# Performance work log

Hardware: AMD Instinct MI355X
Metric: run time of the kernel (lower is better)

## Reference

```python
import jax, jax.numpy as jnp
import numpy as np
import math

B, C, H, W = 16, 256, 32, 32
MPHI = 16      # GRModule projection channels
NNODE = 20     # symbol nodes
DEMB = 300     # fastText dim


def setup_inputs() -> dict:
    key = jax.random.key(0)
    ks = jax.random.split(key, 24)
    r = lambda i, shp, s=0.05: jax.random.normal(ks[i], shp, dtype=jnp.float32) * s
    return {
        'x': r(0, (B, C, H, W), 1.0),
        'emb': r(1, (NNODE, DEMB), 1.0),
        'adj': jax.random.uniform(ks[2], (NNODE, NNODE), dtype=jnp.float32),
        'wq': r(3, (DEMB, DEMB)), 'bq': r(4, (DEMB,)),
        'wk': r(5, (DEMB, DEMB)), 'bk': r(6, (DEMB,)),
        'wv': r(7, (DEMB, DEMB)), 'bv': r(8, (DEMB,)),
        'wo': r(9, (DEMB, DEMB)), 'bo': r(10, (DEMB,)),
        'phi_w': r(11, (MPHI, C)), 'phi_b': r(12, (MPHI,)),
        'glob_w': r(13, (MPHI, C)),
        'gc1_w': r(14, (DEMB, C)),
        'gc2_w': r(15, (C, C)),
        'gw_w': r(16, (C, C)),
        's2l_w': r(17, (2 * C,)), 's2l_b': r(18, (1,)),
        'final_w': r(19, (C, 2 * C)),
    }


def _attention_graph(node, wq, bq, wk, bk, wv, bv, wo, bo):
    # node: [N, 300]. Single-head self-attention, mean-pooled residual (dropout=eval).
    q = node @ wq + bq
    k = node @ wk + bk
    v = node @ wv + bv
    att = jax.nn.softmax(q @ k.T / math.sqrt(DEMB), axis=-1)
    node1 = (att @ v).mean(axis=0, keepdims=True)      # [1, 300]
    node2 = node1 @ wo + bo
    return node + node2                                 # broadcast residual


def _gr_module(x, phi_w, phi_b, glob_w):
    # x: [B, C, H, W] -> [B, HW, C]
    b = x.shape[0]
    phi = jnp.einsum('oc,bchw->bohw', phi_w, x) + phi_b[None, :, None, None]  # [B,16,H,W]
    x_phi = jax.nn.relu(phi.reshape(b, -1, MPHI))       # raw reshape, as in torch .view
    x_phi_T = jax.nn.relu(phi.reshape(b, MPHI, -1))
    g = jnp.einsum('oc,bc->bo', glob_w, x.mean(axis=(2, 3)))  # [B,16]
    # sigmoid of the diag-embedded matrix: off-diagonal becomes sigmoid(0)=0.5 (faithful)
    Dg = jax.nn.sigmoid(jax.vmap(jnp.diag)(g))          # [B,16,16]
    A = jax.nn.softmax(jnp.einsum('bpm,bmn,bnq->bpq', x_phi, Dg, x_phi_T), axis=-1)
    d = 1.0 / jnp.sqrt(A.sum(axis=2))
    d = jnp.where(jnp.isfinite(d), d, 0.0)              # nan/inf -> 0
    L = jnp.eye(A.shape[1], dtype=A.dtype) - d[:, :, None] * A * d[:, None, :]
    return jnp.einsum('bpq,bqc->bpc', L, x.reshape(b, -1, x.shape[1]))


def _normalize_adjacency(adj):
    a_hat = adj + jnp.eye(adj.shape[0], dtype=adj.dtype)
    d = 1.0 / jnp.sqrt(a_hat.sum(axis=1))
    d = jnp.where(jnp.isfinite(d), d, 0.0)
    return d[:, None] * a_hat * d[None, :]


def reference(x, emb, adj, wq, bq, wk, bk, wv, bv, wo, bo,
              phi_w, phi_b, glob_w, gc1_w, gc2_w, gw_w, s2l_w, s2l_b, final_w):
    b, c, h, w = x.shape
    # --- semantic branch: attention over word graph + 2-layer GCN ---
    ev = _attention_graph(emb, wq, bq, wk, bk, wv, bv, wo, bo)  # [N,300]
    ev = jnp.broadcast_to(ev[None], (b, NNODE, DEMB))
    adj_n = _normalize_adjacency(adj)                   # [N,N]
    g1 = jax.nn.relu(jnp.einsum('pq,bqd->bpd', adj_n, ev @ gc1_w))   # [B,N,256]
    g2 = jax.nn.relu(jnp.einsum('pq,bqd->bpd', adj_n, g1 @ gc2_w))   # [B,N,256]
    # --- local branch: GRModule Laplacian smoothing + 1x1 conv ---
    spiral = _gr_module(x, phi_w, phi_b, glob_w)        # [B,HW,C]
    spiral_map = spiral.reshape(b, h, w, c).transpose(0, 3, 1, 2)    # [B,C,H,W]
    local = jnp.einsum('oc,bchw->bohw', gw_w, spiral_map)
    # --- semantic-to-local mapping (1x1 conv over concat == two dot products) ---
    inp_flat = x.transpose(0, 2, 3, 1).reshape(b, h * w, c)          # [B,HW,C]
    w_in, w_ev = s2l_w[:c], s2l_w[c:]
    logits = (inp_flat @ w_in)[:, :, None] + (g2 @ w_ev)[:, None, :] + s2l_b[0]
    mapping = jax.nn.softmax(logits, axis=1)            # softmax over pixels
    app = jax.nn.relu(jnp.einsum('bpm,bmc->bpc', mapping, g2))       # [B,HW,C]
    app = app.reshape(b, h, w, c).transpose(0, 3, 1, 2)              # [B,C,H,W]
    # --- fuse ---
    fused = jnp.concatenate([local, app], axis=1)       # [B,2C,H,W]
    out = jnp.einsum('oc,bchw->bohw', final_w, fused)
    return jax.nn.relu(out + x)
```

## Files before the change

kernel.cpp:

```cpp
#include <hip/hip_runtime.h>
#include <hip/hip_bf16.h>

typedef __bf16 bf16_t;
typedef bf16_t bf16x8 __attribute__((ext_vector_type(8)));
typedef bf16_t bf16x4 __attribute__((ext_vector_type(4)));
typedef float  f32x4  __attribute__((ext_vector_type(4)));

#define MFMA(a,b,c) __builtin_amdgcn_mfma_f32_16x16x32_bf16((a),(b),(c),0,0,0)

__global__ __launch_bounds__(256) void k_front(
    const float* final_w, const float* gw_w, const float* emb,
    const float* wq, const float* bq, const float* wk, const float* bk,
    const float* wv, const float* bvv, const float* x,
    const float* phi_w, const float* phi_b, const float* s2l_w,
    const float* gc1_w, const float* wo, const float* bo,
    bf16_t* M16, float* qkv, bf16_t* fB, bf16_t* fBT, float* s_raw,
    float* xsump, float* csum, float* fmaxp, float* cmaxp, bf16_t* xT,
    float* E1, float* WG1, float* bg1) {
  __shared__ __align__(16) char sp[27648];
  int bid = blockIdx.x, t = threadIdx.x;
  if (bid < 256) {
    float* fw = (float*)sp;
    int o = bid, c = t;
    fw[c] = final_w[o*512 + c];
    __syncthreads();
    float acc = 0.f;
    for (int k = 0; k < 256; ++k) acc += fw[k] * gw_w[k*256 + c];
    M16[o*256 + c] = (bf16_t)acc;
    return;
  }
  if (bid < 316) {
    int id = bid - 256;
    int mat = id / 20, row = id % 20;
    const float* W  = mat == 0 ? wq : (mat == 1 ? wk : wv);
    const float* Bb = mat == 0 ? bq : (mat == 1 ? bk : bvv);
    float* er = (float*)sp;
    for (int i = t; i < 300; i += 256) er[i] = emb[row*300 + i];
    __syncthreads();
    for (int o = t; o < 300; o += 256) {
      float acc = Bb[o];
      for (int d = 0; d < 300; ++d) acc += er[d] * W[d*300 + o];
      qkv[(mat*20 + row)*300 + o] = acc;
    }
    return;
  }
  if (bid < 444) {
    int id = bid - 316;
    int b = id >> 3, role = id & 7;
    const float* xb = x + b*262144;
    float* pw = (float*)sp;
    float* wi = pw + 4096;
    float* pb = wi + 256;
    float* phs = pb + 16;
    unsigned* fmu = (unsigned*)(phs + 2304);
    unsigned* cmu = fmu + 16;
    for (int i = t; i < 4096; i += 256) pw[i] = phi_w[i];
    wi[t] = s2l_w[t];
    if (t < 16) { pb[t] = phi_b[t]; fmu[t] = 0u; }
    if (t == 0) cmu[0] = 0u;
    __syncthreads();
    int hwl = t & 127, half = t >> 7;
    int hw = role*128 + hwl;
    float ph[16];
    #pragma unroll
    for (int o = 0; o < 16; ++o) ph[o] = 0.f;
    float sacc = 0.f;
    for (int ci = 0; ci < 128; ++ci) {
      int c = half*128 + ci;
      float xv = xb[c*1024 + hw];
      sacc += wi[c] * xv;
      #pragma unroll
      for (int o = 0; o < 16; ++o) ph[o] += pw[o*256 + c] * xv;
    }
    if (half == 0) {
      #pragma unroll
      for (int o = 0; o < 16; ++o) phs[hwl*18 + o] = ph[o];
      phs[hwl*18 + 16] = sacc;
    }
    __syncthreads();
    if (half == 1) {
      #pragma unroll
      for (int o = 0; o < 16; ++o) phs[hwl*18 + o] += ph[o];
      s_raw[b*1024 + hw] = phs[hwl*18 + 16] + sacc;
    }
    __syncthreads();
    float csacc = 0.f;
    #pragma unroll
    for (int i = 0; i < 8; ++i) {
      int j = i*256 + t;
      int o = j >> 7, hl = j & 127;
      float val = fmaxf(phs[hl*18 + o] + pb[o], 0.f);
      bf16_t bv16 = (bf16_t)val;
      atomicMax(&fmu[o], __float_as_uint((float)bv16));
      fB [b*16384 + o*1024 + role*128 + hl] = bv16;
      fBT[b*16384 + (role*128 + hl)*16 + o] = bv16;
      csacc += (float)bv16;
    }
    if (half == 0) phs[hwl*18 + 17] = csacc;
    __syncthreads();
    if (half == 1) {
      float cs = phs[hwl*18 + 17] + csacc;
      csum[b*1024 + hw] = cs;
      atomicMax(cmu, __float_as_uint(cs));
    }
    if (t < 16) fmaxp[b*128 + role*16 + t] = __uint_as_float(fmu[t]);
    __syncthreads();
    if (t == 0) cmaxp[b*8 + role] = __uint_as_float(cmu[0]);
    {
      const f32x4* xr = (const f32x4*)(xb + t*1024 + role*128);
      float s4 = 0.f;
      #pragma unroll
      for (int j = 0; j < 32; ++j) { f32x4 v = xr[j]; s4 += v[0] + v[1] + v[2] + v[3]; }
      xsump[(b*8 + role)*256 + t] = s4;
    }
    return;
  }
  if (bid < 464) {
    int n = bid - 444;
    float* er = (float*)sp;
    for (int i = t; i < 300; i += 256) er[i] = emb[n*300 + i];
    __syncthreads();
    float acc = 0.f;
    for (int d = 0; d < 300; ++d) acc += er[d] * gc1_w[d*256 + t];
    E1[n*256 + t] = acc;
    return;
  }
  if (bid < 765) {
    int d0 = bid - 464;
    float* er = (float*)sp;
    if (d0 < 300) { for (int i = t; i < 300; i += 256) er[i] = wo[d0*300 + i]; }
    else          { for (int i = t; i < 300; i += 256) er[i] = bo[i]; }
    __syncthreads();
    float acc = 0.f;
    for (int e = 0; e < 300; ++e) acc += er[e] * gc1_w[e*256 + t];
    if (d0 < 300) WG1[d0*256 + t] = acc; else bg1[t] = acc;
    return;
  }
  {
    int id = bid - 765;
    int bb = id >> 6, tile = id & 63;
    int q0 = (tile >> 2) * 64, c0 = (tile & 3) * 64;
    bf16_t* tl = (bf16_t*)sp;
    const float* xbb = x + bb*262144;
    #pragma unroll
    for (int k = 0; k < 16; ++k) {
      int idx = k*256 + t, qi = idx >> 6, ci = idx & 63;
      tl[ci*74 + qi] = (bf16_t)xbb[(q0 + qi)*256 + c0 + ci];
    }
    __syncthreads();
    #pragma unroll
    for (int k = 0; k < 16; ++k) {
      int idx = k*256 + t, ci = idx >> 6, qi = idx & 63;
      xT[bb*262144 + (c0 + ci)*1024 + q0 + qi] = tl[ci*74 + qi];
    }
    return;
  }
}

__global__ __launch_bounds__(512) void k_mid1(
    const float* adj, const float* qkv, const float* E1,
    const float* glob_w, const float* xsump, const float* s_raw,
    const float* fmaxp, const float* cmaxp,
    float* n1g, float* adjng, float* rsAg, float* AE1g,
    float* dgd, float* mcol, float* fmaxb, float* cmaxb) {
  __shared__ __align__(16) float sp[12480];
  int t = threadIdx.x;
  if (blockIdx.x == 0) {
    float* A  = sp;
    float* Bs = A + 6000;
    float* att  = Bs + 6000;
    float* wsum = att + 400;
    for (int i = t; i < 6000; i += 512) { A[i] = qkv[i]; Bs[i] = qkv[6000 + i]; }
    __syncthreads();
    if (t < 400) {
      int i = t / 20, j = t % 20;
      float acc = 0.f;
      for (int d = 0; d < 300; ++d) acc += A[i*300 + d] * Bs[j*300 + d];
      att[t] = acc * 0.05773502691896258f;
    }
    __syncthreads();
    if (t < 20) {
      float m = -1e30f;
      for (int j = 0; j < 20; ++j) m = fmaxf(m, att[t*20 + j]);
      float s = 0.f;
      for (int j = 0; j < 20; ++j) { float e = __expf(att[t*20 + j] - m); att[t*20 + j] = e; s += e; }
      float inv = 1.f / s;
      for (int j = 0; j < 20; ++j) att[t*20 + j] *= inv;
    }
    __syncthreads();
    if (t < 20) {
      float s = 0.f;
      for (int i = 0; i < 20; ++i) s += att[i*20 + t];
      wsum[t] = s * 0.05f;
    }
    __syncthreads();
    if (t < 300) {
      const float* v = qkv + 12000;
      float acc = 0.f;
      for (int j = 0; j < 20; ++j) acc += wsum[j] * v[j*300 + t];
      n1g[t] = acc;
    }
    return;
  }
  if (blockIdx.x == 1) {
    float* drt = sp;
    float* an  = sp + 32;
    if (t < 20) {
      float s = 1.f;
      for (int j = 0; j < 20; ++j) s += adj[t*20 + j];
      drt[t] = rsqrtf(s);
    }
    __syncthreads();
    if (t < 400) {
      int i = t / 20, j = t % 20;
      float a = adj[t] + (i == j ? 1.f : 0.f);
      float v = drt[i] * a * drt[j];
      an[t] = v;
      adjng[t] = v;
    }
    __syncthreads();
    if (t < 20) {
      float s = 0.f;
      for (int m = 0; m < 20; ++m) s += an[t*20 + m];
      rsAg[t] = s;
    }
    if (t < 256) {
      float e[20];
      #pragma unroll
      for (int m = 0; m < 20; ++m) e[m] = E1[m*256 + t];
      for (int n = 0; n < 20; ++n) {
        float acc = 0.f;
        #pragma unroll
        for (int m = 0; m < 20; ++m) acc += an[n*20 + m] * e[m];
        AE1g[n*256 + t] = acc;
      }
    }
    return;
  }
  int b = blockIdx.x - 2;
  float* xm = sp;
  float* redm = xm + 256;
  float* reds = redm + 8;
  if (t < 256) {
    float s = 0.f;
    #pragma unroll
    for (int r = 0; r < 8; ++r) s += xsump[(b*8 + r)*256 + t];
    xm[t] = s * (1.f / 1024.f);
  }
  if (t >= 256 && t < 272) {
    int m = t - 256; float fm = 0.f;
    for (int r = 0; r < 8; ++r) fm = fmaxf(fm, fmaxp[b*128 + r*16 + m]);
    fmaxb[b*16 + m] = fm;
  }
  if (t == 272) {
    float cm = 0.f;
    for (int r = 0; r < 8; ++r) cm = fmaxf(cm, cmaxp[b*8 + r]);
    cmaxb[b] = cm;
  }
  __syncthreads();
  if (t < 16) {
    float g = 0.f;
    for (int c = 0; c < 256; ++c) g += glob_w[t*256 + c] * xm[c];
    dgd[b*16 + t] = 0.5f * tanhf(0.5f * g);
  }
  float v0 = s_raw[b*1024 + t], v1 = s_raw[b*1024 + 512 + t];
  float m = fmaxf(v0, v1);
  #pragma unroll
  for (int off = 32; off; off >>= 1) m = fmaxf(m, __shfl_xor(m, off, 64));
  int wv = t >> 6, ll = t & 63;
  if (ll == 0) redm[wv] = m;
  __syncthreads();
  float bm = redm[0];
  #pragma unroll
  for (int i = 1; i < 8; ++i) bm = fmaxf(bm, redm[i]);
  float e0 = __expf(v0 - bm), e1 = __expf(v1 - bm);
  float s2 = e0 + e1;
  #pragma unroll
  for (int off = 32; off; off >>= 1) s2 += __shfl_xor(s2, off, 64);
  if (ll == 0) reds[wv] = s2;
  __syncthreads();
  float tot = 0.f;
  #pragma unroll
  for (int i = 0; i < 8; ++i) tot += reds[i];
  float inv = 1.f / tot;
  mcol[b*1024 + t]       = e0 * inv;
  mcol[b*1024 + 512 + t] = e1 * inv;
}

__global__ __launch_bounds__(256) void k_w1(const float* n1g, const float* WG1,
                                            float* w1part) {
  int t = threadIdx.x, i = blockIdx.x, d0 = i*8;
  float acc = 0.f;
  #pragma unroll
  for (int k = 0; k < 8; ++k) {
    int d = d0 + k;
    if (d < 300) acc += n1g[d] * WG1[d*256 + t];
  }
  w1part[i*256 + t] = acc;
}

__global__ __launch_bounds__(256) void k_gu(const float* w1part,
    const float* bg1, const float* AE1g, const float* rsAg, const float* adjng,
    const float* gc2_w, const float* final_w, float* upart) {
  __shared__ float adjns[400], rsAs[32], w1s[256], h2s[176], rgs[8];
  __shared__ float g1s[20*260];
  __shared__ float gs2[2048];
  int t = threadIdx.x, c0 = blockIdx.x * 8;
  for (int i = t; i < 400; i += 256) adjns[i] = adjng[i];
  if (t < 20) rsAs[t] = rsAg[t];
  #pragma unroll
  for (int k2 = 0; k2 < 8; ++k2) {
    int idx = k2*256 + t, d = idx >> 3, cl = idx & 7;
    gs2[idx] = gc2_w[d*256 + c0 + cl];
  }
  {
    float acc = bg1[t];
    #pragma unroll
    for (int i = 0; i < 38; ++i) acc += w1part[i*256 + t];
    w1s[t] = acc;
  }
  float ae[20];
  #pragma unroll
  for (int k2 = 0; k2 < 20; ++k2) ae[k2] = AE1g[k2*256 + t];
  __syncthreads();
  #pragma unroll
  for (int k2 = 0; k2 < 20; ++k2)
    g1s[k2*260 + t] = fmaxf(ae[k2] + rsAs[k2] * w1s[t], 0.f);
  __syncthreads();
  int cl = t & 7, n = t >> 3;
  if (n < 20) {
    float acc = 0.f;
    for (int d = 0; d < 256; ++d) acc += g1s[n*260 + d] * gs2[d*8 + cl];
    h2s[n*8 + cl] = acc;
  }
  __syncthreads();
  if (t < 8) {
    float rga = 0.f;
    for (int nn = 0; nn < 20; ++nn) {
      float a2 = 0.f;
      #pragma unroll
      for (int m = 0; m < 20; ++m) a2 += adjns[nn*20 + m] * h2s[m*8 + t];
      rga += fmaxf(a2, 0.f);
    }
    rgs[t] = rga;
  }
  __syncthreads();
  {
    float acc = 0.f;
    const float* fw = final_w + t*512 + 256 + c0;
    #pragma unroll
    for (int kk = 0; kk < 8; ++kk) acc += fw[kk] * rgs[kk];
    upart[blockIdx.x*256 + t] = acc;
  }
}

__global__ __launch_bounds__(256) void k_main(const float* x, const bf16_t* fB,
    const bf16_t* fBT, const bf16_t* xT, const bf16_t* M16, const float* fmaxb,
    const float* mcol, const float* upart, const float* dgd, const float* csum,
    const float* cmaxb, float* out) {
  int flat = blockIdx.y * 32 + blockIdx.x;
  int b  = (flat & 7) * 2 + ((flat >> 3) >> 5);
  int p0 = ((flat >> 3) & 31) * 32;
  int t = threadIdx.x, w = t >> 6, l = t & 63, lr = l & 15, quad = l >> 4;
  int ph = w & 1, ch = w >> 1;
  __shared__ __align__(16) char smem[16896];
  bf16_t* e_s  = (bf16_t*)smem;
  bf16_t* T_ls = (bf16_t*)smem;
  __shared__ float Mb_s[32], fmax_s[16], u_s[256], dgd_s[16];
  __shared__ float c_s[1024], ha_s[32];
  const float*  xb   = x   + b*262144;
  const bf16_t* fBb  = fB  + b*16384;
  const bf16_t* fBTb = fBT + b*16384;
  const bf16_t* xTb  = xT  + b*262144;
  for (int i = t; i < 1280; i += 256) e_s[i] = (bf16_t)0.f;
  {
    float us = 0.f;
    #pragma unroll
    for (int j = 0; j < 32; ++j) us += upart[j*256 + t];
    u_s[t] = us;
  }
  for (int i = t; i < 1024; i += 256) c_s[i] = csum[b*1024 + i];
  if (t < 16) { fmax_s[t] = fmaxb[b*16 + t]; dgd_s[t] = dgd[b*16 + t]; }
  __syncthreads();
  for (int i = t; i < 512; i += 256) {
    int p = i >> 4, m = i & 15;
    e_s[p*40 + m] = (bf16_t)((float)fBb[p0*16 + i] * dgd_s[m]);
  }
  __syncthreads();
  if (t < 32) {
    float a = 0.f;
    #pragma unroll
    for (int m = 0; m < 16; ++m) a += (float)fBb[(p0 + t)*16 + m];
    float ha = 0.5f * a;
    ha_s[t] = ha;
    float mb = ha * cmaxb[b];
    #pragma unroll
    for (int m = 0; m < 16; ++m) mb += fmaxf((float)e_s[t*40 + m], 0.f) * fmax_s[m];
    Mb_s[t] = mb;
  }
  __syncthreads();
  bf16x8 be = *(const bf16x8*)(e_s + (ph*16 + lr)*40 + quad*8);
  float mb_lane = Mb_s[ph*16 + lr];
  float ha_lane = ha_s[ph*16 + lr];
  float rs = 0.f;
  f32x4 acc[8];
  #pragma unroll
  for (int j = 0; j < 8; ++j) acc[j] = (f32x4){0.f, 0.f, 0.f, 0.f};
  bf16x8 zer;
  #pragma unroll
  for (int j = 0; j < 8; ++j) zer[j] = (bf16_t)0.f;
  const bf16_t* xrow = xTb + (ch*128 + lr)*1024 + quad*8;
  int srcLo = ((quad & 1) << 5) + lr;
  int srcHi = srcLo + 16;
  bool hi = quad >= 2;
  for (int st = 0; st < 32; ++st) {
    bf16x8 a0 = zer, a1 = zer;
    if (quad < 2) {
      a0 = *(const bf16x8*)(fBTb + (st*32 + lr)*16 + quad*8);
      a1 = *(const bf16x8*)(fBTb + (st*32 + 16 + lr)*16 + quad*8);
    }
    bf16x8 bv[8];
    #pragma unroll
    for (int cf = 0; cf < 8; ++cf)
      bv[cf] = *(const bf16x8*)(xrow + cf*16384 + st*32);
    f32x4 z = {0.f, 0.f, 0.f, 0.f};
    f32x4 s0 = MFMA(a0, be, z);
    f32x4 s1 = MFMA(a1, be, z);
    float E0[4], E1v[4];
    #pragma unroll
    for (int r = 0; r < 4; ++r) {
      float S0 = s0[r] + ha_lane * c_s[st*32 + quad*4 + r];
      float S1 = s1[r] + ha_lane * c_s[st*32 + 16 + quad*4 + r];
      E0[r] = __expf(S0 - mb_lane);
      E1v[r] = __expf(S1 - mb_lane);
      rs += E0[r] + E1v[r];
    }
    unsigned P0, P1, P2, P3;
    {
      union { bf16_t h[2]; unsigned u; } pk;
      pk.h[0] = (bf16_t)E0[0];  pk.h[1] = (bf16_t)E0[1];  P0 = pk.u;
      pk.h[0] = (bf16_t)E0[2];  pk.h[1] = (bf16_t)E0[3];  P1 = pk.u;
      pk.h[0] = (bf16_t)E1v[0]; pk.h[1] = (bf16_t)E1v[1]; P2 = pk.u;
      pk.h[0] = (bf16_t)E1v[2]; pk.h[1] = (bf16_t)E1v[3]; P3 = pk.u;
    }
    unsigned xA = (unsigned)__shfl((int)P0, srcLo, 64);
    unsigned xB = (unsigned)__shfl((int)P2, srcLo, 64);
    unsigned yA = (unsigned)__shfl((int)P1, srcLo, 64);
    unsigned yB = (unsigned)__shfl((int)P3, srcLo, 64);
    unsigned zA = (unsigned)__shfl((int)P0, srcHi, 64);
    unsigned zB = (unsigned)__shfl((int)P2, srcHi, 64);
    unsigned wA = (unsigned)__shfl((int)P1, srcHi, 64);
    unsigned wB = (unsigned)__shfl((int)P3, srcHi, 64);
    union { unsigned u[4]; bf16x8 v; } af;
    af.u[0] = hi ? xB : xA;
    af.u[1] = hi ? yB : yA;
    af.u[2] = hi ? zB : zA;
    af.u[3] = hi ? wB : wA;
    bf16x8 ap = af.v;
    #pragma unroll
    for (int cf = 0; cf < 8; ++cf) acc[cf] = MFMA(ap, bv[cf], acc[cf]);
  }
  rs += __shfl_xor(rs, 16, 64);
  rs += __shfl_xor(rs, 32, 64);
  float rsinv = 1.f / fmaxf(rs, 1e-30f);
  float rsv[4];
  #pragma unroll
  for (int r = 0; r < 4; ++r) rsv[r] = __shfl(rsinv, quad*4 + r, 64);
  __syncthreads();
  #pragma unroll
  for (int cf = 0; cf < 8; ++cf)
    #pragma unroll
    for (int r = 0; r < 4; ++r) {
      int p = ph*16 + quad*4 + r;
      int c = ch*128 + cf*16 + lr;
      float tv = xb[(p0 + p)*256 + c] - acc[cf][r] * rsv[r];
      T_ls[p*264 + c] = (bf16_t)tv;
    }
  __syncthreads();
  f32x4 acc2[4][2];
  #pragma unroll
  for (int i = 0; i < 4; ++i)
    #pragma unroll
    for (int j = 0; j < 2; ++j) acc2[i][j] = (f32x4){0.f, 0.f, 0.f, 0.f};
  for (int c0 = 0; c0 < 256; c0 += 32) {
    bf16x8 am[4], bt[2];
    #pragma unroll
    for (int of = 0; of < 4; ++of)
      am[of] = *(const bf16x8*)(M16 + (w*64 + of*16 + lr)*256 + c0 + quad*8);
    #pragma unroll
    for (int pf = 0; pf < 2; ++pf)
      bt[pf] = *(const bf16x8*)(T_ls + (pf*16 + lr)*264 + c0 + quad*8);
    #pragma unroll
    for (int of = 0; of < 4; ++of)
      #pragma unroll
      for (int pf = 0; pf < 2; ++pf) acc2[of][pf] = MFMA(am[of], bt[pf], acc2[of][pf]);
  }
  float* outb = out + b*262144;
  #pragma unroll
  for (int of = 0; of < 4; ++of)
    #pragma unroll
    for (int pf = 0; pf < 2; ++pf)
      #pragma unroll
      for (int r = 0; r < 4; ++r) {
        int o = w*64 + of*16 + quad*4 + r;
        int pg = p0 + pf*16 + lr;
        float v = acc2[of][pf][r] + mcol[b*1024 + pg] * u_s[o] + xb[o*1024 + pg];
        outb[o*1024 + pg] = fmaxf(v, 0.f);
      }
}


extern "C" void kernel_launch(void* const* d_in, const int* in_sizes, int n_in,
                              void* d_out, int out_size, void* d_ws, size_t ws_size,
                              hipStream_t stream) {
  (void)in_sizes; (void)n_in; (void)out_size; (void)ws_size;
  const float* x       = (const float*)d_in[0];
  const float* emb     = (const float*)d_in[1];
  const float* adj     = (const float*)d_in[2];
  const float* wq      = (const float*)d_in[3];
  const float* bq      = (const float*)d_in[4];
  const float* wk      = (const float*)d_in[5];
  const float* bk      = (const float*)d_in[6];
  const float* wv      = (const float*)d_in[7];
  const float* bv      = (const float*)d_in[8];
  const float* wo      = (const float*)d_in[9];
  const float* bo      = (const float*)d_in[10];
  const float* phi_w   = (const float*)d_in[11];
  const float* phi_b   = (const float*)d_in[12];
  const float* glob_w  = (const float*)d_in[13];
  const float* gc1_w   = (const float*)d_in[14];
  const float* gc2_w   = (const float*)d_in[15];
  const float* gw_w    = (const float*)d_in[16];
  const float* s2l_w   = (const float*)d_in[17];
  const float* final_w = (const float*)d_in[19];
  float* out = (float*)d_out;

  float* W = (float*)d_ws;
  float* qkv    = W + 0;
  float* xsump  = W + 18048;
  float* s_raw  = W + 50816;
  float* mcol   = W + 67200;
  float* fmaxb  = W + 83584;
  float* dgd    = W + 83840;
  float* csum   = W + 84096;
  float* cmaxb  = W + 100480;
  float* fmaxp  = W + 100544;
  float* cmaxp  = W + 102592;
  float* E1     = W + 102720;
  float* WG1    = W + 107840;
  float* bg1    = W + 184640;
  float* n1     = W + 184896;
  float* adjn   = W + 185216;
  float* rsA    = W + 185664;
  float* AE1    = W + 185728;
  float* upart  = W + 190848;
  float* w1part = W + 199040;
  bf16_t* M16 = (bf16_t*)((char*)d_ws + 851968);
  bf16_t* fB  = (bf16_t*)((char*)d_ws + 983040);
  bf16_t* fBT = (bf16_t*)((char*)d_ws + 1507328);
  bf16_t* xT  = (bf16_t*)((char*)d_ws + 2031616);

  k_front<<<1789, 256, 0, stream>>>(final_w, gw_w, emb, wq, bq, wk, bk, wv, bv, x,
                                    phi_w, phi_b, s2l_w, gc1_w, wo, bo,
                                    M16, qkv, fB, fBT, s_raw, xsump, csum,
                                    fmaxp, cmaxp, xT, E1, WG1, bg1);
  k_mid1<<<18, 512, 0, stream>>>(adj, qkv, E1, glob_w, xsump, s_raw,
                                 fmaxp, cmaxp,
                                 n1, adjn, rsA, AE1, dgd, mcol, fmaxb, cmaxb);
  k_w1<<<38, 256, 0, stream>>>(n1, WG1, w1part);
  k_gu<<<32, 256, 0, stream>>>(w1part, bg1, AE1, rsA, adjn, gc2_w, final_w, upart);
  k_main<<<dim3(32, 16), 256, 0, stream>>>(x, fB, fBT, xT, M16, fmaxb, mcol, upart,
                                           dgd, csum, cmaxb, out);
}
```

Measured before the change: 228.9 us.

## Halve k_main pixel tile, split key dimension across waves with LDS exchange and prefetch

k_main now processes 16 query pixels per block instead of 32 and launches twice as many blocks. The four waves are split two ways: pairs of waves each compute the exp scores for alternating 32-pixel key chunks, and each wave owns 64 output channels. Scores go through a double-buffered LDS tile with a block barrier each step, replacing the cross-lane shuffle exchange. The next step's fBT and xT operands are prefetched into registers. The aim is more blocks for occupancy and less per-block work, at the cost of a __syncthreads per key step, a cross-wave row-sum reduction, and reloading M16 and xT in twice as many blocks.

```diff
diff --git a/kernel.cpp b/kernel.cpp
--- a/kernel.cpp
+++ b/kernel.cpp
@@ -358,21 +358,22 @@
     const bf16_t* fBT, const bf16_t* xT, const bf16_t* M16, const float* fmaxb,
     const float* mcol, const float* upart, const float* dgd, const float* csum,
     const float* cmaxb, float* out) {
-  int flat = blockIdx.y * 32 + blockIdx.x;
-  int b  = (flat & 7) * 2 + ((flat >> 3) >> 5);
-  int p0 = ((flat >> 3) & 31) * 32;
+  int flat = blockIdx.y * 64 + blockIdx.x;
+  int b  = (flat & 7) * 2 + ((flat >> 3) >> 6);
+  int p0 = ((flat >> 3) & 63) * 16;
   int t = threadIdx.x, w = t >> 6, l = t & 63, lr = l & 15, quad = l >> 4;
-  int ph = w & 1, ch = w >> 1;
-  __shared__ __align__(16) char smem[16896];
-  bf16_t* e_s  = (bf16_t*)smem;
+  int ks = w >> 1, qh = w & 1;
+  __shared__ __align__(16) char smem[8448];
+  bf16_t* PT0  = (bf16_t*)smem;
+  bf16_t* e_s  = (bf16_t*)(smem + 5120);
   bf16_t* T_ls = (bf16_t*)smem;
-  __shared__ float Mb_s[32], fmax_s[16], u_s[256], dgd_s[16];
-  __shared__ float c_s[1024], ha_s[32];
+  __shared__ float Mb_s[16], fmax_s[16], u_s[256], rsinv_s[16], dgd_s[16];
+  __shared__ float c_s[1024], ha_s[16], rs_s[4][16];
   const float*  xb   = x   + b*262144;
   const bf16_t* fBb  = fB  + b*16384;
   const bf16_t* fBTb = fBT + b*16384;
   const bf16_t* xTb  = xT  + b*262144;
-  for (int i = t; i < 1280; i += 256) e_s[i] = (bf16_t)0.f;
+  for (int i = t; i < 640; i += 256) e_s[i] = (bf16_t)0.f;
   {
     float us = 0.f;
     #pragma unroll
@@ -382,12 +383,9 @@
   for (int i = t; i < 1024; i += 256) c_s[i] = csum[b*1024 + i];
   if (t < 16) { fmax_s[t] = fmaxb[b*16 + t]; dgd_s[t] = dgd[b*16 + t]; }
   __syncthreads();
-  for (int i = t; i < 512; i += 256) {
-    int p = i >> 4, m = i & 15;
-    e_s[p*40 + m] = (bf16_t)((float)fBb[p0*16 + i] * dgd_s[m]);
-  }
-  __syncthreads();
-  if (t < 32) {
+  e_s[(t >> 4)*40 + (t & 15)] = (bf16_t)((float)fBb[p0*16 + t] * dgd_s[t & 15]);
+  __syncthreads();
+  if (t < 16) {
     float a = 0.f;
     #pragma unroll
     for (int m = 0; m < 16; ++m) a += (float)fBb[(p0 + t)*16 + m];
@@ -399,114 +397,105 @@
     Mb_s[t] = mb;
   }
   __syncthreads();
-  bf16x8 be = *(const bf16x8*)(e_s + (ph*16 + lr)*40 + quad*8);
-  float mb_lane = Mb_s[ph*16 + lr];
-  float ha_lane = ha_s[ph*16 + lr];
+  bf16x8 be = *(const bf16x8*)(e_s + lr*40 + quad*8);
+  float mb_lane = Mb_s[lr];
+  float ha_lane = ha_s[lr];
   float rs = 0.f;
-  f32x4 acc[8];
-  #pragma unroll
-  for (int j = 0; j < 8; ++j) acc[j] = (f32x4){0.f, 0.f, 0.f, 0.f};
+  f32x4 acc[4];
+  #pragma unroll
+  for (int j = 0; j < 4; ++j) acc[j] = (f32x4){0.f, 0.f, 0.f, 0.f};
   bf16x8 zer;
   #pragma unroll
   for (int j = 0; j < 8; ++j) zer[j] = (bf16_t)0.f;
-  const bf16_t* xrow = xTb + (ch*128 + lr)*1024 + quad*8;
-  int srcLo = ((quad & 1) << 5) + lr;
-  int srcHi = srcLo + 16;
-  bool hi = quad >= 2;
-  for (int st = 0; st < 32; ++st) {
-    bf16x8 a0 = zer, a1 = zer;
-    if (quad < 2) {
-      a0 = *(const bf16x8*)(fBTb + (st*32 + lr)*16 + quad*8);
-      a1 = *(const bf16x8*)(fBTb + (st*32 + 16 + lr)*16 + quad*8);
-    }
-    bf16x8 bv[8];
-    #pragma unroll
-    for (int cf = 0; cf < 8; ++cf)
-      bv[cf] = *(const bf16x8*)(xrow + cf*16384 + st*32);
+  bf16x8 a0 = zer, a0n = zer;
+  if (quad < 2) a0 = *(const bf16x8*)(fBTb + (ks*32 + qh*16 + lr)*16 + quad*8);
+  const bf16_t* xrow = xTb + (w*64 + lr)*1024 + quad*8;
+  bf16x8 bv[2][4], bvn[2][4];
+  #pragma unroll
+  for (int k = 0; k < 2; ++k)
+    #pragma unroll
+    for (int cf = 0; cf < 4; ++cf)
+      bv[k][cf] = *(const bf16x8*)(xrow + cf*16384 + k*32);
+  int cur = 0;
+  for (int u2 = 0; u2 < 16; ++u2) {
+    int st = u2*2 + ks;
     f32x4 z = {0.f, 0.f, 0.f, 0.f};
     f32x4 s0 = MFMA(a0, be, z);
-    f32x4 s1 = MFMA(a1, be, z);
-    float E0[4], E1v[4];
+    if (u2 < 15) {
+      if (quad < 2)
+        a0n = *(const bf16x8*)(fBTb + (((u2 + 1)*2 + ks)*32 + qh*16 + lr)*16 + quad*8);
+      #pragma unroll
+      for (int k = 0; k < 2; ++k)
+        #pragma unroll
+        for (int cf = 0; cf < 4; ++cf)
+          bvn[k][cf] = *(const bf16x8*)(xrow + cf*16384 + (u2*2 + 2 + k)*32);
+    }
+    bf16_t* PTc = PT0 + cur*1280;
+    bf16x4 pv;
     #pragma unroll
     for (int r = 0; r < 4; ++r) {
-      float S0 = s0[r] + ha_lane * c_s[st*32 + quad*4 + r];
-      float S1 = s1[r] + ha_lane * c_s[st*32 + 16 + quad*4 + r];
-      E0[r] = __expf(S0 - mb_lane);
-      E1v[r] = __expf(S1 - mb_lane);
-      rs += E0[r] + E1v[r];
-    }
-    unsigned P0, P1, P2, P3;
-    {
-      union { bf16_t h[2]; unsigned u; } pk;
-      pk.h[0] = (bf16_t)E0[0];  pk.h[1] = (bf16_t)E0[1];  P0 = pk.u;
-      pk.h[0] = (bf16_t)E0[2];  pk.h[1] = (bf16_t)E0[3];  P1 = pk.u;
-      pk.h[0] = (bf16_t)E1v[0]; pk.h[1] = (bf16_t)E1v[1]; P2 = pk.u;
-      pk.h[0] = (bf16_t)E1v[2]; pk.h[1] = (bf16_t)E1v[3]; P3 = pk.u;
-    }
-    unsigned xA = (unsigned)__shfl((int)P0, srcLo, 64);
-    unsigned xB = (unsigned)__shfl((int)P2, srcLo, 64);
-    unsigned yA = (unsigned)__shfl((int)P1, srcLo, 64);
-    unsigned yB = (unsigned)__shfl((int)P3, srcLo, 64);
-    unsigned zA = (unsigned)__shfl((int)P0, srcHi, 64);
-    unsigned zB = (unsigned)__shfl((int)P2, srcHi, 64);
-    unsigned wA = (unsigned)__shfl((int)P1, srcHi, 64);
-    unsigned wB = (unsigned)__shfl((int)P3, srcHi, 64);
-    union { unsigned u[4]; bf16x8 v; } af;
-    af.u[0] = hi ? xB : xA;
-    af.u[1] = hi ? yB : yA;
-    af.u[2] = hi ? zB : zA;
-    af.u[3] = hi ? wB : wA;
-    bf16x8 ap = af.v;
-    #pragma unroll
-    for (int cf = 0; cf < 8; ++cf) acc[cf] = MFMA(ap, bv[cf], acc[cf]);
+      float S0 = s0[r] + ha_lane * c_s[st*32 + qh*16 + quad*4 + r];
+      float E0 = __expf(S0 - mb_lane);
+      rs += E0; pv[r] = (bf16_t)E0;
+    }
+    *(bf16x4*)(PTc + ks*640 + lr*40 + qh*16 + quad*4) = pv;
+    __syncthreads();
+    bf16x8 ap0 = *(const bf16x8*)(PTc + lr*40 + quad*8);
+    bf16x8 ap1 = *(const bf16x8*)(PTc + 640 + lr*40 + quad*8);
+    #pragma unroll
+    for (int cf = 0; cf < 4; ++cf) {
+      acc[cf] = MFMA(ap0, bv[0][cf], acc[cf]);
+      acc[cf] = MFMA(ap1, bv[1][cf], acc[cf]);
+    }
+    if (u2 < 15) {
+      a0 = a0n;
+      #pragma unroll
+      for (int k = 0; k < 2; ++k)
+        #pragma unroll
+        for (int cf = 0; cf < 4; ++cf) bv[k][cf] = bvn[k][cf];
+    }
+    cur ^= 1;
   }
   rs += __shfl_xor(rs, 16, 64);
   rs += __shfl_xor(rs, 32, 64);
-  float rsinv = 1.f / fmaxf(rs, 1e-30f);
-  float rsv[4];
-  #pragma unroll
-  for (int r = 0; r < 4; ++r) rsv[r] = __shfl(rsinv, quad*4 + r, 64);
-  __syncthreads();
-  #pragma unroll
-  for (int cf = 0; cf < 8; ++cf)
+  if (l < 16) rs_s[w][l] = rs;
+  __syncthreads();
+  if (t < 16) rsinv_s[t] =
+      1.f / fmaxf(rs_s[0][t] + rs_s[1][t] + rs_s[2][t] + rs_s[3][t], 1e-30f);
+  __syncthreads();
+  #pragma unroll
+  for (int cf = 0; cf < 4; ++cf)
     #pragma unroll
     for (int r = 0; r < 4; ++r) {
-      int p = ph*16 + quad*4 + r;
-      int c = ch*128 + cf*16 + lr;
-      float tv = xb[(p0 + p)*256 + c] - acc[cf][r] * rsv[r];
+      int p = quad*4 + r;
+      int c = w*64 + cf*16 + lr;
+      float tv = xb[(p0 + p)*256 + c] - acc[cf][r] * rsinv_s[p];
       T_ls[p*264 + c] = (bf16_t)tv;
     }
   __syncthreads();
-  f32x4 acc2[4][2];
-  #pragma unroll
-  for (int i = 0; i < 4; ++i)
-    #pragma unroll
-    for (int j = 0; j < 2; ++j) acc2[i][j] = (f32x4){0.f, 0.f, 0.f, 0.f};
+  f32x4 acc2[4];
+  #pragma unroll
+  for (int i = 0; i < 4; ++i) acc2[i] = (f32x4){0.f, 0.f, 0.f, 0.f};
   for (int c0 = 0; c0 < 256; c0 += 32) {
-    bf16x8 am[4], bt[2];
+    bf16x8 am[4];
     #pragma unroll
     for (int of = 0; of < 4; ++of)
       am[of] = *(const bf16x8*)(M16 + (w*64 + of*16 + lr)*256 + c0 + quad*8);
-    #pragma unroll
-    for (int pf = 0; pf < 2; ++pf)
-      bt[pf] = *(const bf16x8*)(T_ls + (pf*16 + lr)*264 + c0 + quad*8);
-    #pragma unroll
-    for (int of = 0; of < 4; ++of)
-      #pragma unroll
-      for (int pf = 0; pf < 2; ++pf) acc2[of][pf] = MFMA(am[of], bt[pf], acc2[of][pf]);
-  }
+    bf16x8 bt = *(const bf16x8*)(T_ls + lr*264 + c0 + quad*8);
+    #pragma unroll
+    for (int of = 0; of < 4; ++of) acc2[of] = MFMA(am[of], bt, acc2[of]);
+  }
+  float mc = mcol[b*1024 + p0 + lr];
   float* outb = out + b*262144;
   #pragma unroll
   for (int of = 0; of < 4; ++of)
     #pragma unroll
-    for (int pf = 0; pf < 2; ++pf)
-      #pragma unroll
-      for (int r = 0; r < 4; ++r) {
-        int o = w*64 + of*16 + quad*4 + r;
-        int pg = p0 + pf*16 + lr;
-        float v = acc2[of][pf][r] + mcol[b*1024 + pg] * u_s[o] + xb[o*1024 + pg];
-        outb[o*1024 + pg] = fmaxf(v, 0.f);
-      }
+    for (int r = 0; r < 4; ++r) {
+      int o = w*64 + of*16 + quad*4 + r;
+      int pg = p0 + lr;
+      float v = acc2[of][r] + mc * u_s[o] + xb[o*1024 + pg];
+      outb[o*1024 + pg] = fmaxf(v, 0.f);
+    }
 }
 
 
@@ -569,6 +558,6 @@
                                  n1, adjn, rsA, AE1, dgd, mcol, fmaxb, cmaxb);
   k_w1<<<38, 256, 0, stream>>>(n1, WG1, w1part);
   k_gu<<<32, 256, 0, stream>>>(w1part, bg1, AE1, rsA, adjn, gc2_w, final_w, upart);
-  k_main<<<dim3(32, 16), 256, 0, stream>>>(x, fB, fBT, xT, M16, fmaxb, mcol, upart,
+  k_main<<<dim3(64, 16), 256, 0, stream>>>(x, fB, fBT, xT, M16, fmaxb, mcol, upart,
                                            dgd, csum, cmaxb, out);
 }
```

Measured after the change: 238.3 us. 4.1% more time.
